# Performance work log

Hardware: AMD Instinct MI355X
Metric: run time of the kernel (lower is better)

## Reference

```python
import jax, jax.numpy as jnp
import numpy as np

B, S, D = 8, 512, 512
H, DK = 64, 8          # 64 heads hardcoded in SelfAttentiveLBLBiLM
WIDTH = 16             # local window width
NL = 2                 # highway layers
N = S + 2 * WIDTH      # padded sequence length


def setup_inputs() -> dict:
    key = jax.random.key(0)
    ks = jax.random.split(key, 12)
    s = 0.02
    return {
        "inputs": jax.random.normal(ks[0], (B, S, D), jnp.float32),
        "left_pad": jax.random.normal(ks[1], (WIDTH, D), jnp.float32) * s,
        "right_pad": jax.random.normal(ks[2], (WIDTH, D), jnp.float32) * s,
        "l_Wqkv": jax.random.normal(ks[3], (3, D, D), jnp.float32) * s,
        "l_bqkv": jnp.zeros((3, D), jnp.float32),
        "l_Wo": jax.random.normal(ks[4], (D, D), jnp.float32) * s,
        "l_bo": jnp.zeros((D,), jnp.float32),
        "r_Wqkv": jax.random.normal(ks[5], (3, D, D), jnp.float32) * s,
        "r_bqkv": jnp.zeros((3, D), jnp.float32),
        "r_Wo": jax.random.normal(ks[6], (D, D), jnp.float32) * s,
        "r_bo": jnp.zeros((D,), jnp.float32),
        "lhw_W": jax.random.normal(ks[7], (NL, 2 * D, D), jnp.float32) * s,
        "lhw_b": jnp.zeros((NL, 2 * D), jnp.float32),
        "rhw_W": jax.random.normal(ks[8], (NL, 2 * D, D), jnp.float32) * s,
        "rhw_b": jnp.zeros((NL, 2 * D), jnp.float32),
    }


def _masks(n, width):
    i = jnp.arange(n)[:, None]
    j = jnp.arange(n)[None, :]
    # local_mask: triu(k=-width-1) * (1 - triu(k=1)) -> i-width-1 <= j <= i
    left = (j <= i) & (j >= i - width - 1)
    # right mask is the full flip of the left mask
    right = (j >= i) & (j <= i + width + 1)
    return left, right


def _mha(x, Wqkv, bqkv, Wo, bo, mask):
    b, n, d = x.shape
    # torch Linear: y = x @ W.T + b, W is [out, in]
    qkv = jnp.einsum("bnd,tod->tbno", x, Wqkv) + bqkv[:, None, None, :]
    q, k, v = [t.reshape(b, n, H, DK).transpose(0, 2, 1, 3) for t in qkv]
    scores = jnp.einsum("bhqd,bhkd->bhqk", q, k) / jnp.sqrt(jnp.float32(DK))
    scores = jnp.where(mask[None, None], scores, jnp.float32(-1e9))
    p = jax.nn.softmax(scores, axis=-1)
    out = jnp.einsum("bhqk,bhkd->bhqd", p, v)
    out = out.transpose(0, 2, 1, 3).reshape(b, n, d)
    return out @ Wo.T + bo


def _highway(x, Ws, bs):
    for l in range(NL):
        proj = x @ Ws[l].T + bs[l]
        nonlin = jax.nn.relu(proj[..., :D])
        gate = jax.nn.sigmoid(proj[..., D:])
        x = gate * x + (1.0 - gate) * nonlin
    return x


def reference(inputs, left_pad, right_pad, l_Wqkv, l_bqkv, l_Wo, l_bo,
              r_Wqkv, r_bqkv, r_Wo, r_bo, lhw_W, lhw_b, rhw_W, rhw_b):
    b = inputs.shape[0]
    new_inputs = jnp.concatenate(
        [jnp.broadcast_to(left_pad[None], (b, WIDTH, D)), inputs,
         jnp.broadcast_to(right_pad[None], (b, WIDTH, D))], axis=1)  # [B, N, D]
    left_mask, right_mask = _masks(N, WIDTH)
    new_left = _mha(new_inputs, l_Wqkv, l_bqkv, l_Wo, l_bo, left_mask)
    new_right = _mha(new_inputs, r_Wqkv, r_bqkv, r_Wo, r_bo, right_mask)
    # per-step loop indexes position start + width -> slice [WIDTH : WIDTH + S]
    left_out = _highway(new_left[:, WIDTH:WIDTH + S], lhw_W, lhw_b)
    right_out = _highway(new_right[:, WIDTH:WIDTH + S], rhw_W, rhw_b)
    last = jnp.concatenate([left_out, right_out], axis=-1)  # [B, S, 2D]
    all_layers = last[None]  # [1, B, S, 2D] (single layer stacked on dim 0)
    return (all_layers, last)
```

## Files before the change

kernel.cpp:

```cpp
#include <hip/hip_runtime.h>
#include <math.h>

#define B_ 8
#define S_ 512
#define D_ 512
#define WIDTH_ 16
#define NSEQ 544
#define MROWS 4352
#define MOUT 4096
#define OUTHALF 4194304

typedef _Float16 half8 __attribute__((ext_vector_type(8)));
typedef _Float16 half4 __attribute__((ext_vector_type(4)));
typedef float floatx4 __attribute__((ext_vector_type(4)));

#define GLD16(g, l) __builtin_amdgcn_global_load_lds(                          \
    (const __attribute__((address_space(1))) void*)(g),                        \
    (__attribute__((address_space(3))) void*)(l), 16, 0, 0)

__device__ __forceinline__ float sigmoidf_(float x) {
    return 1.f / (1.f + __expf(-x));
}

__global__ __launch_bounds__(256)
void gemm_qkv(const _Float16* __restrict__ A,
              const _Float16* __restrict__ B0, const _Float16* __restrict__ B1,
              const float* __restrict__ bias0, const float* __restrict__ bias1,
              _Float16* __restrict__ C16) {
    const int lda = 512, ldb = 512, ldc = 1536, K = 512;
    __shared__ _Float16 As[128 * 32];
    __shared__ _Float16 Bs[128 * 32];
    const int t    = threadIdx.x;
    const int wave = t >> 6;
    const int lane = t & 63;
    const int bm = blockIdx.y * 128;
    const int bn = blockIdx.x * 128;
    const int z  = blockIdx.z;
    const _Float16* B = z ? B1 : B0;
    const float* bias = z ? bias1 : bias0;
    _Float16* C = C16 + (size_t)z * MROWS * 1536;
    const int wm = (wave & 1) * 64;
    const int wn = (wave >> 1) * 64;

    const int inst = wave * 2;
    const int r0 = inst * 16 + (lane >> 2);
    const int kf = (lane & 3) * 8;

    const _Float16* Ag0 = A + (size_t)(bm + r0) * lda + kf;
    const _Float16* Ag1 = Ag0 + (size_t)16 * lda;
    const _Float16* Bg0 = B + (size_t)(bn + r0) * ldb + kf;
    const _Float16* Bg1 = Bg0 + (size_t)16 * ldb;
    _Float16* As0 = &As[inst * 512];
    _Float16* As1 = As0 + 512;
    _Float16* Bs0 = &Bs[inst * 512];
    _Float16* Bs1 = Bs0 + 512;

    const int fr = lane & 15;
    const int fq = (lane >> 4) * 8;

    floatx4 acc[4][4] = {};

    for (int k0 = 0; k0 < K; k0 += 32) {
        GLD16(Ag0, As0); GLD16(Ag1, As1);
        GLD16(Bg0, Bs0); GLD16(Bg1, Bs1);
        Ag0 += 32; Ag1 += 32; Bg0 += 32; Bg1 += 32;
        __syncthreads();
        half8 af[4], bf[4];
#pragma unroll
        for (int s = 0; s < 4; s++) {
            af[s] = *(const half8*)&As[(wm + s * 16 + fr) * 32 + fq];
            bf[s] = *(const half8*)&Bs[(wn + s * 16 + fr) * 32 + fq];
        }
#pragma unroll
        for (int i = 0; i < 4; i++)
#pragma unroll
            for (int j = 0; j < 4; j++)
                acc[i][j] = __builtin_amdgcn_mfma_f32_16x16x32_f16(
                    af[i], bf[j], acc[i][j], 0, 0, 0);
        __syncthreads();
    }

    const int rq = (lane >> 4) * 4;
    const int cc = lane & 15;
#pragma unroll
    for (int i = 0; i < 4; i++) {
        const int rbase = bm + wm + i * 16 + rq;
#pragma unroll
        for (int j = 0; j < 4; j++) {
            const int col = bn + wn + j * 16 + cc;
            const float bv = bias[col];
#pragma unroll
            for (int r = 0; r < 4; r++)
                C[(size_t)(rbase + r) * ldc + col] = (_Float16)(acc[i][j][r] + bv);
        }
    }
}

__global__ __launch_bounds__(256)
void gemm_wo(const _Float16* __restrict__ Aall,
             const _Float16* __restrict__ B0, const _Float16* __restrict__ B1,
             const float* __restrict__ bias0, const float* __restrict__ bias1,
             _Float16* __restrict__ x16base) {
    const int lda = 512, ldb = 512, K = 512;
    __shared__ _Float16 As[64 * 32];
    __shared__ _Float16 Bs[128 * 32];
    const int t    = threadIdx.x;
    const int wave = t >> 6;
    const int lane = t & 63;
    const int bm = blockIdx.y * 64;
    const int bn = blockIdx.x * 128;
    const int z  = blockIdx.z;
    const _Float16* A = Aall + (size_t)z * MROWS * 512;
    const _Float16* B = z ? B1 : B0;
    const float* bias = z ? bias1 : bias0;
    _Float16* x16 = x16base + (size_t)z * MOUT * 512;

    const int wm = (wave & 1) * 32;
    const int wn = (wave >> 1) * 64;

    const int rA = wave * 16 + (lane >> 2);
    const int rB = wave * 32 + (lane >> 2);
    const int kf = (lane & 3) * 8;

    const _Float16* Ag0 = A + (size_t)(bm + rA) * lda + kf;
    const _Float16* Bg0 = B + (size_t)(bn + rB) * ldb + kf;
    const _Float16* Bg1 = Bg0 + (size_t)16 * ldb;
    _Float16* As0 = &As[wave * 512];
    _Float16* Bs0 = &Bs[wave * 1024];
    _Float16* Bs1 = Bs0 + 512;

    const int fr = lane & 15;
    const int fq = (lane >> 4) * 8;

    floatx4 acc[2][4] = {};

    for (int k0 = 0; k0 < K; k0 += 32) {
        GLD16(Ag0, As0);
        GLD16(Bg0, Bs0); GLD16(Bg1, Bs1);
        Ag0 += 32; Bg0 += 32; Bg1 += 32;
        __syncthreads();
        half8 af[2], bf[4];
#pragma unroll
        for (int s = 0; s < 2; s++)
            af[s] = *(const half8*)&As[(wm + s * 16 + fr) * 32 + fq];
#pragma unroll
        for (int s = 0; s < 4; s++)
            bf[s] = *(const half8*)&Bs[(wn + s * 16 + fr) * 32 + fq];
#pragma unroll
        for (int i = 0; i < 2; i++)
#pragma unroll
            for (int j = 0; j < 4; j++)
                acc[i][j] = __builtin_amdgcn_mfma_f32_16x16x32_f16(
                    af[i], bf[j], acc[i][j], 0, 0, 0);
        __syncthreads();
    }

    const int rq = (lane >> 4) * 4;
    const int cc = lane & 15;
#pragma unroll
    for (int i = 0; i < 2; i++) {
        const int rbase = bm + wm + i * 16 + rq;
#pragma unroll
        for (int r = 0; r < 4; r++) {
            const int row = rbase + r;
            const int b = row / NSEQ;
            const int s = row - b * NSEQ;
            if (s < WIDTH_ || s >= WIDTH_ + S_) continue;
            const int m = b * S_ + s - WIDTH_;
#pragma unroll
            for (int j = 0; j < 4; j++) {
                const int col = bn + wn + j * 16 + cc;
                x16[(size_t)m * 512 + col] = (_Float16)(acc[i][j][r] + bias[col]);
            }
        }
    }
}

__global__ __launch_bounds__(256)
void gemm_hw(const _Float16* __restrict__ x16inbase,
             const _Float16* __restrict__ W0, const _Float16* __restrict__ W1,
             const float* __restrict__ b0, const float* __restrict__ b1,
             _Float16* __restrict__ x16outbase,
             float* __restrict__ outlastbase,
             float* __restrict__ outallbase) {
    const int lda = 512, ldb = 512, K = 512;
    __shared__ _Float16 As[128 * 32];
    __shared__ _Float16 Bn[64 * 32];
    __shared__ _Float16 Bg[64 * 32];
    const int t    = threadIdx.x;
    const int wave = t >> 6;
    const int lane = t & 63;
    const int bm = blockIdx.y * 128;
    const int bn = blockIdx.x * 64;
    const int z  = blockIdx.z;
    const _Float16* A = x16inbase + (size_t)z * MOUT * 512;
    const _Float16* W = z ? W1 : W0;
    const float* bias = z ? b1 : b0;
    _Float16* x16out = x16outbase ? x16outbase + (size_t)z * MOUT * 512 : nullptr;

    const int wm = (wave & 1) * 64;
    const int wn = (wave >> 1) * 32;

    const int rA = wave * 32 + (lane >> 2);
    const int rB = wave * 16 + (lane >> 2);
    const int kf = (lane & 3) * 8;

    const _Float16* Ag0 = A + (size_t)(bm + rA) * lda + kf;
    const _Float16* Ag1 = Ag0 + (size_t)16 * lda;
    const _Float16* Bn0 = W + (size_t)(bn + rB) * ldb + kf;
    const _Float16* Bg0 = W + (size_t)(512 + bn + rB) * ldb + kf;
    _Float16* As0  = &As[wave * 1024];
    _Float16* As1  = As0 + 512;
    _Float16* Bns0 = &Bn[wave * 512];
    _Float16* Bgs0 = &Bg[wave * 512];

    const int fr = lane & 15;
    const int fq = (lane >> 4) * 8;

    floatx4 accn[4][2] = {};
    floatx4 accg[4][2] = {};

    for (int k0 = 0; k0 < K; k0 += 32) {
        GLD16(Ag0, As0); GLD16(Ag1, As1);
        GLD16(Bn0, Bns0);
        GLD16(Bg0, Bgs0);
        Ag0 += 32; Ag1 += 32; Bn0 += 32; Bg0 += 32;
        __syncthreads();
        half8 af[4], bnf[2], bgf[2];
#pragma unroll
        for (int s = 0; s < 4; s++)
            af[s] = *(const half8*)&As[(wm + s * 16 + fr) * 32 + fq];
#pragma unroll
        for (int s = 0; s < 2; s++) {
            bnf[s] = *(const half8*)&Bn[(wn + s * 16 + fr) * 32 + fq];
            bgf[s] = *(const half8*)&Bg[(wn + s * 16 + fr) * 32 + fq];
        }
#pragma unroll
        for (int i = 0; i < 4; i++)
#pragma unroll
            for (int j = 0; j < 2; j++) {
                accn[i][j] = __builtin_amdgcn_mfma_f32_16x16x32_f16(
                    af[i], bnf[j], accn[i][j], 0, 0, 0);
                accg[i][j] = __builtin_amdgcn_mfma_f32_16x16x32_f16(
                    af[i], bgf[j], accg[i][j], 0, 0, 0);
            }
        __syncthreads();
    }

    float* outlast = outlastbase ? outlastbase + z * 512 : nullptr;
    float* outall  = outallbase  ? outallbase  + z * 512 : nullptr;

    const int rq = (lane >> 4) * 4;
    const int cc = lane & 15;
#pragma unroll
    for (int i = 0; i < 4; i++) {
        const int rbase = bm + wm + i * 16 + rq;
#pragma unroll
        for (int j = 0; j < 2; j++) {
            const int col = bn + wn + j * 16 + cc;
            const float bnl = bias[col];
            const float bgt = bias[512 + col];
#pragma unroll
            for (int r = 0; r < 4; r++) {
                const int row = rbase + r;
                const float nl = fmaxf(accn[i][j][r] + bnl, 0.f);
                const float g  = sigmoidf_(accg[i][j][r] + bgt);
                const float xo = (float)A[(size_t)row * 512 + col];
                const float v  = g * xo + (1.f - g) * nl;
                if (x16out) {
                    x16out[(size_t)row * 512 + col] = (_Float16)v;
                } else {
                    outlast[(size_t)row * 1024 + col] = v;
                    outall[(size_t)row * 1024 + col] = v;
                }
            }
        }
    }
}

__global__ __launch_bounds__(256)
void attn_win(const _Float16* __restrict__ qkvall, _Float16* __restrict__ attall) {
    const int dir = blockIdx.y;
    const int dlo = dir ? 0 : -(WIDTH_ + 1);
    const _Float16* qkv = qkvall + (size_t)dir * MROWS * 1536;
    _Float16* att = attall + (size_t)dir * MROWS * 512;
    const int tid = blockIdx.x * 256 + threadIdx.x;
    const int h  = tid & 63;
    const int bi = tid >> 6;
    const int i  = bi % NSEQ;
    const int b  = bi / NSEQ;
    const int j0 = i + dlo;
    const float scale = 0.35355339059327373f;

    const half8 q8 = *(const half8*)(qkv + (size_t)bi * 1536 + h * 8);
    float q[8];
#pragma unroll
    for (int d = 0; d < 8; d++) q[d] = (float)q8[d];

    float s[18];
    float mx = -1e30f;
#pragma unroll
    for (int jj = 0; jj < 18; jj++) {
        const int j = j0 + jj;
        const int jc = j < 0 ? 0 : (j > NSEQ - 1 ? NSEQ - 1 : j);
        const half8 k8 = *(const half8*)(qkv + (size_t)(b * NSEQ + jc) * 1536 + 512 + h * 8);
        float d = 0.f;
#pragma unroll
        for (int dd = 0; dd < 8; dd++) d = fmaf(q[dd], (float)k8[dd], d);
        s[jj] = (j == jc) ? d * scale : -1e30f;
        mx = fmaxf(mx, s[jj]);
    }
    float sum = 0.f;
#pragma unroll
    for (int jj = 0; jj < 18; jj++) { s[jj] = __expf(s[jj] - mx); sum += s[jj]; }
    const float inv = 1.f / sum;

    float o[8] = {};
#pragma unroll
    for (int jj = 0; jj < 18; jj++) {
        const int j = j0 + jj;
        const int jc = j < 0 ? 0 : (j > NSEQ - 1 ? NSEQ - 1 : j);
        const half8 v8 = *(const half8*)(qkv + (size_t)(b * NSEQ + jc) * 1536 + 1024 + h * 8);
        const float p = s[jj];
#pragma unroll
        for (int dd = 0; dd < 8; dd++) o[dd] = fmaf(p, (float)v8[dd], o[dd]);
    }
    half8 o16;
#pragma unroll
    for (int d = 0; d < 8; d++) o16[d] = (_Float16)(o[d] * inv);
    *(half8*)&att[(size_t)bi * 512 + h * 8] = o16;
}

__global__ void prep(const float* __restrict__ lq, const float* __restrict__ rq,
                     const float* __restrict__ lo, const float* __restrict__ ro,
                     const float* __restrict__ lh, const float* __restrict__ rh,
                     _Float16* __restrict__ wdst,
                     const float* __restrict__ inp,
                     const float* __restrict__ lp,
                     const float* __restrict__ rp,
                     _Float16* __restrict__ padX) {
    const int gb = blockIdx.x;
    if (gb < 4096) {
        int idx = gb * 256 + threadIdx.x;
        const float* src; int off;
        if      (idx < 196608) { src = lq; off = idx; }
        else if (idx < 393216) { src = rq; off = idx - 196608; }
        else if (idx < 458752) { src = lo; off = idx - 393216; }
        else if (idx < 524288) { src = ro; off = idx - 458752; }
        else if (idx < 786432) { src = lh; off = idx - 524288; }
        else                   { src = rh; off = idx - 786432; }
        const float4 v = ((const float4*)src)[off];
        half4 h = { (_Float16)v.x, (_Float16)v.y, (_Float16)v.z, (_Float16)v.w };
        ((half4*)wdst)[idx] = h;
    } else {
        int idx = (gb - 4096) * 256 + threadIdx.x;
        const int c4 = idx & 127;
        const int t  = idx >> 7;
        const int n = t % NSEQ;
        const int b = t / NSEQ;
        const float* src;
        if (n < WIDTH_)            src = lp + n * 512;
        else if (n < WIDTH_ + S_)  src = inp + ((size_t)(b * S_ + n - WIDTH_)) * 512;
        else                       src = rp + (n - WIDTH_ - S_) * 512;
        const float4 v = *(const float4*)(src + c4 * 4);
        half4 h = { (_Float16)v.x, (_Float16)v.y, (_Float16)v.z, (_Float16)v.w };
        *(half4*)&padX[(size_t)t * 512 + c4 * 4] = h;
    }
}

extern "C" void kernel_launch(void* const* d_in, const int* in_sizes, int n_in,
                              void* d_out, int out_size, void* d_ws, size_t ws_size,
                              hipStream_t stream) {
    const float* inputs    = (const float*)d_in[0];
    const float* left_pad  = (const float*)d_in[1];
    const float* right_pad = (const float*)d_in[2];
    const float* l_Wqkv = (const float*)d_in[3];
    const float* l_bqkv = (const float*)d_in[4];
    const float* l_Wo   = (const float*)d_in[5];
    const float* l_bo   = (const float*)d_in[6];
    const float* r_Wqkv = (const float*)d_in[7];
    const float* r_bqkv = (const float*)d_in[8];
    const float* r_Wo   = (const float*)d_in[9];
    const float* r_bo   = (const float*)d_in[10];
    const float* lhw_W  = (const float*)d_in[11];
    const float* lhw_b  = (const float*)d_in[12];
    const float* rhw_W  = (const float*)d_in[13];
    const float* rhw_b  = (const float*)d_in[14];

    float* out = (float*)d_out;
    _Float16* h = (_Float16*)d_ws;

    _Float16* padX16 = h;
    _Float16* w16    = h + 2228224;
    _Float16* lqkv16 = w16;
    _Float16* rqkv16 = w16 + 786432;
    _Float16* lWo16  = w16 + 1572864;
    _Float16* rWo16  = w16 + 1835008;
    _Float16* lhw16  = w16 + 2097152;
    _Float16* rhw16  = w16 + 3145728;
    _Float16* qkv16  = h + 6422528;
    _Float16* att16  = h + 19791872;
    _Float16* x16a   = h + 24248320;
    _Float16* x16b   = h + 28442624;

    float* out_all  = out;
    float* out_last = out + OUTHALF;

    prep<<<6272, 256, 0, stream>>>(l_Wqkv, r_Wqkv, l_Wo, r_Wo, lhw_W, rhw_W, w16,
                                   inputs, left_pad, right_pad, padX16);

    gemm_qkv<<<dim3(12, 34, 2), 256, 0, stream>>>(
        padX16, lqkv16, rqkv16, l_bqkv, r_bqkv, qkv16);

    attn_win<<<dim3(MROWS * 64 / 256, 2), 256, 0, stream>>>(qkv16, att16);

    gemm_wo<<<dim3(4, 68, 2), 256, 0, stream>>>(
        att16, lWo16, rWo16, l_bo, r_bo, x16a);

    gemm_hw<<<dim3(8, 32, 2), 256, 0, stream>>>(
        x16a, lhw16, rhw16, lhw_b, rhw_b, x16b, nullptr, nullptr);
    gemm_hw<<<dim3(8, 32, 2), 256, 0, stream>>>(
        x16b, lhw16 + 524288, rhw16 + 524288, lhw_b + 1024, rhw_b + 1024,
        nullptr, out_last, out_all);
}
```

Measured before the change: 220.6 us.

## Fuse all stages into a persistent megakernel with grid-wide barriers

Replaces the six separate kernel launches with one persistent kernel of 512 blocks that loops over each stage's work items and separates stages with a software global barrier built on atomics. This is meant to remove launch overhead and the idle gaps between kernels. In exchange, each stage is now limited to 512 resident blocks, which reduces parallelism for stages that had more blocks. The barrier assumes all blocks are co-resident and adds spin-wait cost, and a memset is added to reset the barrier counter.

New measurement: 712.5 us. 3.23x slower.

```diff
diff --git a/kernel.cpp b/kernel.cpp
--- a/kernel.cpp
+++ b/kernel.cpp
@@ -9,6 +9,7 @@
 #define MROWS 4352
 #define MOUT 4096
 #define OUTHALF 4194304
+#define NBLK 512
 
 typedef _Float16 half8 __attribute__((ext_vector_type(8)));
 typedef _Float16 half4 __attribute__((ext_vector_type(4)));
@@ -22,404 +23,435 @@
     return 1.f / (1.f + __expf(-x));
 }
 
-__global__ __launch_bounds__(256)
-void gemm_qkv(const _Float16* __restrict__ A,
-              const _Float16* __restrict__ B0, const _Float16* __restrict__ B1,
-              const float* __restrict__ bias0, const float* __restrict__ bias1,
-              _Float16* __restrict__ C16) {
+struct Args {
+    const float *inputs, *left_pad, *right_pad;
+    const float *l_Wqkv, *l_bqkv, *l_Wo, *l_bo;
+    const float *r_Wqkv, *r_bqkv, *r_Wo, *r_bo;
+    const float *lhw_W, *lhw_b, *rhw_W, *rhw_b;
+    _Float16 *padX16, *w16;
+    _Float16 *lqkv16, *rqkv16, *lWo16, *rWo16, *lhw16, *rhw16;
+    _Float16 *qkv16, *att16, *x16a, *x16b;
+    float *out_all, *out_last;
+    int *bar;
+};
+
+__device__ __forceinline__ void gsync(int* bar, int tid) {
+    __syncthreads();
+    if (tid == 0) {
+        int* cnt = bar;
+        int* gen = bar + 1;
+        const int g = __hip_atomic_load(gen, __ATOMIC_RELAXED, __HIP_MEMORY_SCOPE_AGENT);
+        const int prev = __hip_atomic_fetch_add(cnt, 1, __ATOMIC_ACQ_REL, __HIP_MEMORY_SCOPE_AGENT);
+        if (prev == NBLK - 1) {
+            __hip_atomic_store(cnt, 0, __ATOMIC_RELAXED, __HIP_MEMORY_SCOPE_AGENT);
+            __hip_atomic_fetch_add(gen, 1, __ATOMIC_RELEASE, __HIP_MEMORY_SCOPE_AGENT);
+        } else {
+            while (__hip_atomic_load(gen, __ATOMIC_ACQUIRE, __HIP_MEMORY_SCOPE_AGENT) == g)
+                __builtin_amdgcn_s_sleep(8);
+        }
+    }
+    __syncthreads();
+}
+
+__device__ __forceinline__ void prep_phase(const Args& a, int pb, int tid) {
+    for (int gb = pb; gb < 6272; gb += NBLK) {
+        if (gb < 4096) {
+            int idx = gb * 256 + tid;
+            const float* src; int off;
+            if      (idx < 196608) { src = a.l_Wqkv; off = idx; }
+            else if (idx < 393216) { src = a.r_Wqkv; off = idx - 196608; }
+            else if (idx < 458752) { src = a.l_Wo;   off = idx - 393216; }
+            else if (idx < 524288) { src = a.r_Wo;   off = idx - 458752; }
+            else if (idx < 786432) { src = a.lhw_W;  off = idx - 524288; }
+            else                   { src = a.rhw_W;  off = idx - 786432; }
+            const float4 v = ((const float4*)src)[off];
+            half4 h = { (_Float16)v.x, (_Float16)v.y, (_Float16)v.z, (_Float16)v.w };
+            ((half4*)a.w16)[idx] = h;
+        } else {
+            int idx = (gb - 4096) * 256 + tid;
+            const int c4 = idx & 127;
+            const int t  = idx >> 7;
+            const int n = t % NSEQ;
+            const int b = t / NSEQ;
+            const float* src;
+            if (n < WIDTH_)            src = a.left_pad + n * 512;
+            else if (n < WIDTH_ + S_)  src = a.inputs + ((size_t)(b * S_ + n - WIDTH_)) * 512;
+            else                       src = a.right_pad + (n - WIDTH_ - S_) * 512;
+            const float4 v = *(const float4*)(src + c4 * 4);
+            half4 h = { (_Float16)v.x, (_Float16)v.y, (_Float16)v.z, (_Float16)v.w };
+            *(half4*)&a.padX16[(size_t)t * 512 + c4 * 4] = h;
+        }
+    }
+}
+
+__device__ __forceinline__ void qkv_phase(const Args& a, int pb, int tid,
+                                          _Float16* As, _Float16* Bs) {
     const int lda = 512, ldb = 512, ldc = 1536, K = 512;
-    __shared__ _Float16 As[128 * 32];
-    __shared__ _Float16 Bs[128 * 32];
-    const int t    = threadIdx.x;
-    const int wave = t >> 6;
-    const int lane = t & 63;
-    const int bm = blockIdx.y * 128;
-    const int bn = blockIdx.x * 128;
-    const int z  = blockIdx.z;
-    const _Float16* B = z ? B1 : B0;
-    const float* bias = z ? bias1 : bias0;
-    _Float16* C = C16 + (size_t)z * MROWS * 1536;
-    const int wm = (wave & 1) * 64;
-    const int wn = (wave >> 1) * 64;
-
-    const int inst = wave * 2;
-    const int r0 = inst * 16 + (lane >> 2);
-    const int kf = (lane & 3) * 8;
-
-    const _Float16* Ag0 = A + (size_t)(bm + r0) * lda + kf;
-    const _Float16* Ag1 = Ag0 + (size_t)16 * lda;
-    const _Float16* Bg0 = B + (size_t)(bn + r0) * ldb + kf;
-    const _Float16* Bg1 = Bg0 + (size_t)16 * ldb;
-    _Float16* As0 = &As[inst * 512];
-    _Float16* As1 = As0 + 512;
-    _Float16* Bs0 = &Bs[inst * 512];
-    _Float16* Bs1 = Bs0 + 512;
-
-    const int fr = lane & 15;
-    const int fq = (lane >> 4) * 8;
-
-    floatx4 acc[4][4] = {};
-
-    for (int k0 = 0; k0 < K; k0 += 32) {
-        GLD16(Ag0, As0); GLD16(Ag1, As1);
-        GLD16(Bg0, Bs0); GLD16(Bg1, Bs1);
-        Ag0 += 32; Ag1 += 32; Bg0 += 32; Bg1 += 32;
-        __syncthreads();
-        half8 af[4], bf[4];
-#pragma unroll
-        for (int s = 0; s < 4; s++) {
-            af[s] = *(const half8*)&As[(wm + s * 16 + fr) * 32 + fq];
-            bf[s] = *(const half8*)&Bs[(wn + s * 16 + fr) * 32 + fq];
-        }
-#pragma unroll
-        for (int i = 0; i < 4; i++)
-#pragma unroll
-            for (int j = 0; j < 4; j++)
-                acc[i][j] = __builtin_amdgcn_mfma_f32_16x16x32_f16(
-                    af[i], bf[j], acc[i][j], 0, 0, 0);
-        __syncthreads();
-    }
-
-    const int rq = (lane >> 4) * 4;
-    const int cc = lane & 15;
-#pragma unroll
-    for (int i = 0; i < 4; i++) {
-        const int rbase = bm + wm + i * 16 + rq;
-#pragma unroll
-        for (int j = 0; j < 4; j++) {
-            const int col = bn + wn + j * 16 + cc;
-            const float bv = bias[col];
-#pragma unroll
-            for (int r = 0; r < 4; r++)
-                C[(size_t)(rbase + r) * ldc + col] = (_Float16)(acc[i][j][r] + bv);
-        }
-    }
-}
-
-__global__ __launch_bounds__(256)
-void gemm_wo(const _Float16* __restrict__ Aall,
-             const _Float16* __restrict__ B0, const _Float16* __restrict__ B1,
-             const float* __restrict__ bias0, const float* __restrict__ bias1,
-             _Float16* __restrict__ x16base) {
-    const int lda = 512, ldb = 512, K = 512;
-    __shared__ _Float16 As[64 * 32];
-    __shared__ _Float16 Bs[128 * 32];
-    const int t    = threadIdx.x;
-    const int wave = t >> 6;
-    const int lane = t & 63;
-    const int bm = blockIdx.y * 64;
-    const int bn = blockIdx.x * 128;
-    const int z  = blockIdx.z;
-    const _Float16* A = Aall + (size_t)z * MROWS * 512;
-    const _Float16* B = z ? B1 : B0;
-    const float* bias = z ? bias1 : bias0;
-    _Float16* x16 = x16base + (size_t)z * MOUT * 512;
-
-    const int wm = (wave & 1) * 32;
-    const int wn = (wave >> 1) * 64;
-
-    const int rA = wave * 16 + (lane >> 2);
-    const int rB = wave * 32 + (lane >> 2);
-    const int kf = (lane & 3) * 8;
-
-    const _Float16* Ag0 = A + (size_t)(bm + rA) * lda + kf;
-    const _Float16* Bg0 = B + (size_t)(bn + rB) * ldb + kf;
-    const _Float16* Bg1 = Bg0 + (size_t)16 * ldb;
-    _Float16* As0 = &As[wave * 512];
-    _Float16* Bs0 = &Bs[wave * 1024];
-    _Float16* Bs1 = Bs0 + 512;
-
-    const int fr = lane & 15;
-    const int fq = (lane >> 4) * 8;
-
-    floatx4 acc[2][4] = {};
-
-    for (int k0 = 0; k0 < K; k0 += 32) {
-        GLD16(Ag0, As0);
-        GLD16(Bg0, Bs0); GLD16(Bg1, Bs1);
-        Ag0 += 32; Bg0 += 32; Bg1 += 32;
-        __syncthreads();
-        half8 af[2], bf[4];
-#pragma unroll
-        for (int s = 0; s < 2; s++)
-            af[s] = *(const half8*)&As[(wm + s * 16 + fr) * 32 + fq];
-#pragma unroll
-        for (int s = 0; s < 4; s++)
-            bf[s] = *(const half8*)&Bs[(wn + s * 16 + fr) * 32 + fq];
-#pragma unroll
-        for (int i = 0; i < 2; i++)
-#pragma unroll
-            for (int j = 0; j < 4; j++)
-                acc[i][j] = __builtin_amdgcn_mfma_f32_16x16x32_f16(
-                    af[i], bf[j], acc[i][j], 0, 0, 0);
-        __syncthreads();
-    }
-
-    const int rq = (lane >> 4) * 4;
-    const int cc = lane & 15;
-#pragma unroll
-    for (int i = 0; i < 2; i++) {
-        const int rbase = bm + wm + i * 16 + rq;
-#pragma unroll
-        for (int r = 0; r < 4; r++) {
-            const int row = rbase + r;
-            const int b = row / NSEQ;
-            const int s = row - b * NSEQ;
-            if (s < WIDTH_ || s >= WIDTH_ + S_) continue;
-            const int m = b * S_ + s - WIDTH_;
+    const int wave = tid >> 6;
+    const int lane = tid & 63;
+    for (int job = pb; job < 816; job += NBLK) {
+        const int z   = job / 408;
+        const int rem = job % 408;
+        const int bm  = (rem / 12) * 128;
+        const int bn  = (rem % 12) * 128;
+        const _Float16* A = a.padX16;
+        const _Float16* B = z ? a.rqkv16 : a.lqkv16;
+        const float* bias = z ? a.r_bqkv : a.l_bqkv;
+        _Float16* C = a.qkv16 + (size_t)z * MROWS * 1536;
+        const int wm = (wave & 1) * 64;
+        const int wn = (wave >> 1) * 64;
+
+        const int inst = wave * 2;
+        const int r0 = inst * 16 + (lane >> 2);
+        const int kf = (lane & 3) * 8;
+
+        const _Float16* Ag0 = A + (size_t)(bm + r0) * lda + kf;
+        const _Float16* Ag1 = Ag0 + (size_t)16 * lda;
+        const _Float16* Bg0 = B + (size_t)(bn + r0) * ldb + kf;
+        const _Float16* Bg1 = Bg0 + (size_t)16 * ldb;
+        _Float16* As0 = &As[inst * 512];
+        _Float16* As1 = As0 + 512;
+        _Float16* Bs0 = &Bs[inst * 512];
+        _Float16* Bs1 = Bs0 + 512;
+
+        const int fr = lane & 15;
+        const int fq = (lane >> 4) * 8;
+
+        floatx4 acc[4][4] = {};
+
+        for (int k0 = 0; k0 < K; k0 += 32) {
+            GLD16(Ag0, As0); GLD16(Ag1, As1);
+            GLD16(Bg0, Bs0); GLD16(Bg1, Bs1);
+            Ag0 += 32; Ag1 += 32; Bg0 += 32; Bg1 += 32;
+            __syncthreads();
+            half8 af[4], bf[4];
+#pragma unroll
+            for (int s = 0; s < 4; s++) {
+                af[s] = *(const half8*)&As[(wm + s * 16 + fr) * 32 + fq];
+                bf[s] = *(const half8*)&Bs[(wn + s * 16 + fr) * 32 + fq];
+            }
+#pragma unroll
+            for (int i = 0; i < 4; i++)
+#pragma unroll
+                for (int j = 0; j < 4; j++)
+                    acc[i][j] = __builtin_amdgcn_mfma_f32_16x16x32_f16(
+                        af[i], bf[j], acc[i][j], 0, 0, 0);
+            __syncthreads();
+        }
+
+        const int rq = (lane >> 4) * 4;
+        const int cc = lane & 15;
+#pragma unroll
+        for (int i = 0; i < 4; i++) {
+            const int rbase = bm + wm + i * 16 + rq;
 #pragma unroll
             for (int j = 0; j < 4; j++) {
                 const int col = bn + wn + j * 16 + cc;
-                x16[(size_t)m * 512 + col] = (_Float16)(acc[i][j][r] + bias[col]);
+                const float bv = bias[col];
+#pragma unroll
+                for (int r = 0; r < 4; r++)
+                    C[(size_t)(rbase + r) * ldc + col] = (_Float16)(acc[i][j][r] + bv);
             }
         }
     }
 }
 
-__global__ __launch_bounds__(256)
-void gemm_hw(const _Float16* __restrict__ x16inbase,
-             const _Float16* __restrict__ W0, const _Float16* __restrict__ W1,
-             const float* __restrict__ b0, const float* __restrict__ b1,
-             _Float16* __restrict__ x16outbase,
-             float* __restrict__ outlastbase,
-             float* __restrict__ outallbase) {
+__device__ __forceinline__ void attn_phase(const Args& a, int pb, int tid) {
+    for (int job = pb; job < 2176; job += NBLK) {
+        const int dir = job / 1088;
+        const int jx  = job % 1088;
+        const int dlo = dir ? 0 : -(WIDTH_ + 1);
+        const _Float16* qkv = a.qkv16 + (size_t)dir * MROWS * 1536;
+        _Float16* att = a.att16 + (size_t)dir * MROWS * 512;
+        const int t  = jx * 256 + tid;
+        const int h  = t & 63;
+        const int bi = t >> 6;
+        const int i  = bi % NSEQ;
+        const int b  = bi / NSEQ;
+        const int j0 = i + dlo;
+        const float scale = 0.35355339059327373f;
+
+        const half8 q8 = *(const half8*)(qkv + (size_t)bi * 1536 + h * 8);
+        float q[8];
+#pragma unroll
+        for (int d = 0; d < 8; d++) q[d] = (float)q8[d];
+
+        float s[18];
+        float mx = -1e30f;
+#pragma unroll
+        for (int jj = 0; jj < 18; jj++) {
+            const int j = j0 + jj;
+            const int jc = j < 0 ? 0 : (j > NSEQ - 1 ? NSEQ - 1 : j);
+            const half8 k8 = *(const half8*)(qkv + (size_t)(b * NSEQ + jc) * 1536 + 512 + h * 8);
+            float d = 0.f;
+#pragma unroll
+            for (int dd = 0; dd < 8; dd++) d = fmaf(q[dd], (float)k8[dd], d);
+            s[jj] = (j == jc) ? d * scale : -1e30f;
+            mx = fmaxf(mx, s[jj]);
+        }
+        float sum = 0.f;
+#pragma unroll
+        for (int jj = 0; jj < 18; jj++) { s[jj] = __expf(s[jj] - mx); sum += s[jj]; }
+        const float inv = 1.f / sum;
+
+        float o[8] = {};
+#pragma unroll
+        for (int jj = 0; jj < 18; jj++) {
+            const int j = j0 + jj;
+            const int jc = j < 0 ? 0 : (j > NSEQ - 1 ? NSEQ - 1 : j);
+            const half8 v8 = *(const half8*)(qkv + (size_t)(b * NSEQ + jc) * 1536 + 1024 + h * 8);
+            const float p = s[jj];
+#pragma unroll
+            for (int dd = 0; dd < 8; dd++) o[dd] = fmaf(p, (float)v8[dd], o[dd]);
+        }
+        half8 o16;
+#pragma unroll
+        for (int d = 0; d < 8; d++) o16[d] = (_Float16)(o[d] * inv);
+        *(half8*)&att[(size_t)bi * 512 + h * 8] = o16;
+    }
+}
+
+__device__ __forceinline__ void wo_phase(const Args& a, int pb, int tid,
+                                         _Float16* As, _Float16* Bs) {
     const int lda = 512, ldb = 512, K = 512;
-    __shared__ _Float16 As[128 * 32];
-    __shared__ _Float16 Bn[64 * 32];
-    __shared__ _Float16 Bg[64 * 32];
-    const int t    = threadIdx.x;
-    const int wave = t >> 6;
-    const int lane = t & 63;
-    const int bm = blockIdx.y * 128;
-    const int bn = blockIdx.x * 64;
-    const int z  = blockIdx.z;
-    const _Float16* A = x16inbase + (size_t)z * MOUT * 512;
-    const _Float16* W = z ? W1 : W0;
-    const float* bias = z ? b1 : b0;
-    _Float16* x16out = x16outbase ? x16outbase + (size_t)z * MOUT * 512 : nullptr;
-
-    const int wm = (wave & 1) * 64;
-    const int wn = (wave >> 1) * 32;
-
-    const int rA = wave * 32 + (lane >> 2);
-    const int rB = wave * 16 + (lane >> 2);
-    const int kf = (lane & 3) * 8;
-
-    const _Float16* Ag0 = A + (size_t)(bm + rA) * lda + kf;
-    const _Float16* Ag1 = Ag0 + (size_t)16 * lda;
-    const _Float16* Bn0 = W + (size_t)(bn + rB) * ldb + kf;
-    const _Float16* Bg0 = W + (size_t)(512 + bn + rB) * ldb + kf;
-    _Float16* As0  = &As[wave * 1024];
-    _Float16* As1  = As0 + 512;
-    _Float16* Bns0 = &Bn[wave * 512];
-    _Float16* Bgs0 = &Bg[wave * 512];
-
-    const int fr = lane & 15;
-    const int fq = (lane >> 4) * 8;
-
-    floatx4 accn[4][2] = {};
-    floatx4 accg[4][2] = {};
-
-    for (int k0 = 0; k0 < K; k0 += 32) {
-        GLD16(Ag0, As0); GLD16(Ag1, As1);
-        GLD16(Bn0, Bns0);
-        GLD16(Bg0, Bgs0);
-        Ag0 += 32; Ag1 += 32; Bn0 += 32; Bg0 += 32;
-        __syncthreads();
-        half8 af[4], bnf[2], bgf[2];
-#pragma unroll
-        for (int s = 0; s < 4; s++)
-            af[s] = *(const half8*)&As[(wm + s * 16 + fr) * 32 + fq];
-#pragma unroll
-        for (int s = 0; s < 2; s++) {
-            bnf[s] = *(const half8*)&Bn[(wn + s * 16 + fr) * 32 + fq];
-            bgf[s] = *(const half8*)&Bg[(wn + s * 16 + fr) * 32 + fq];
-        }
-#pragma unroll
-        for (int i = 0; i < 4; i++)
-#pragma unroll
-            for (int j = 0; j < 2; j++) {
-                accn[i][j] = __builtin_amdgcn_mfma_f32_16x16x32_f16(
-                    af[i], bnf[j], accn[i][j], 0, 0, 0);
-                accg[i][j] = __builtin_amdgcn_mfma_f32_16x16x32_f16(
-                    af[i], bgf[j], accg[i][j], 0, 0, 0);
-            }
-        __syncthreads();
-    }
-
-    float* outlast = outlastbase ? outlastbase + z * 512 : nullptr;
-    float* outall  = outallbase  ? outallbase  + z * 512 : nullptr;
-
-    const int rq = (lane >> 4) * 4;
-    const int cc = lane & 15;
-#pragma unroll
-    for (int i = 0; i < 4; i++) {
-        const int rbase = bm + wm + i * 16 + rq;
-#pragma unroll
-        for (int j = 0; j < 2; j++) {
-            const int col = bn + wn + j * 16 + cc;
-            const float bnl = bias[col];
-            const float bgt = bias[512 + col];
+    const int wave = tid >> 6;
+    const int lane = tid & 63;
+    for (int job = pb; job < 544; job += NBLK) {
+        const int z   = job / 272;
+        const int rem = job % 272;
+        const int bm  = (rem / 4) * 64;
+        const int bn  = (rem % 4) * 128;
+        const _Float16* A = a.att16 + (size_t)z * MROWS * 512;
+        const _Float16* B = z ? a.rWo16 : a.lWo16;
+        const float* bias = z ? a.r_bo : a.l_bo;
+        _Float16* x16 = a.x16a + (size_t)z * MOUT * 512;
+
+        const int wm = (wave & 1) * 32;
+        const int wn = (wave >> 1) * 64;
+
+        const int rA = wave * 16 + (lane >> 2);
+        const int rB = wave * 32 + (lane >> 2);
+        const int kf = (lane & 3) * 8;
+
+        const _Float16* Ag0 = A + (size_t)(bm + rA) * lda + kf;
+        const _Float16* Bg0 = B + (size_t)(bn + rB) * ldb + kf;
+        const _Float16* Bg1 = Bg0 + (size_t)16 * ldb;
+        _Float16* As0 = &As[wave * 512];
+        _Float16* Bs0 = &Bs[wave * 1024];
+        _Float16* Bs1 = Bs0 + 512;
+
+        const int fr = lane & 15;
+        const int fq = (lane >> 4) * 8;
+
+        floatx4 acc[2][4] = {};
+
+        for (int k0 = 0; k0 < K; k0 += 32) {
+            GLD16(Ag0, As0);
+            GLD16(Bg0, Bs0); GLD16(Bg1, Bs1);
+            Ag0 += 32; Bg0 += 32; Bg1 += 32;
+            __syncthreads();
+            half8 af[2], bf[4];
+#pragma unroll
+            for (int s = 0; s < 2; s++)
+                af[s] = *(const half8*)&As[(wm + s * 16 + fr) * 32 + fq];
+#pragma unroll
+            for (int s = 0; s < 4; s++)
+                bf[s] = *(const half8*)&Bs[(wn + s * 16 + fr) * 32 + fq];
+#pragma unroll
+            for (int i = 0; i < 2; i++)
+#pragma unroll
+                for (int j = 0; j < 4; j++)
+                    acc[i][j] = __builtin_amdgcn_mfma_f32_16x16x32_f16(
+                        af[i], bf[j], acc[i][j], 0, 0, 0);
+            __syncthreads();
+        }
+
+        const int rq = (lane >> 4) * 4;
+        const int cc = lane & 15;
+#pragma unroll
+        for (int i = 0; i < 2; i++) {
+            const int rbase = bm + wm + i * 16 + rq;
 #pragma unroll
             for (int r = 0; r < 4; r++) {
                 const int row = rbase + r;
-                const float nl = fmaxf(accn[i][j][r] + bnl, 0.f);
-                const float g  = sigmoidf_(accg[i][j][r] + bgt);
-                const float xo = (float)A[(size_t)row * 512 + col];
-                const float v  = g * xo + (1.f - g) * nl;
-                if (x16out) {
-                    x16out[(size_t)row * 512 + col] = (_Float16)v;
-                } else {
-                    outlast[(size_t)row * 1024 + col] = v;
-                    outall[(size_t)row * 1024 + col] = v;
+                const int b = row / NSEQ;
+                const int s = row - b * NSEQ;
+                if (s < WIDTH_ || s >= WIDTH_ + S_) continue;
+                const int m = b * S_ + s - WIDTH_;
+#pragma unroll
+                for (int j = 0; j < 4; j++) {
+                    const int col = bn + wn + j * 16 + cc;
+                    x16[(size_t)m * 512 + col] = (_Float16)(acc[i][j][r] + bias[col]);
                 }
             }
         }
     }
 }
 
-__global__ __launch_bounds__(256)
-void attn_win(const _Float16* __restrict__ qkvall, _Float16* __restrict__ attall) {
-    const int dir = blockIdx.y;
-    const int dlo = dir ? 0 : -(WIDTH_ + 1);
-    const _Float16* qkv = qkvall + (size_t)dir * MROWS * 1536;
-    _Float16* att = attall + (size_t)dir * MROWS * 512;
-    const int tid = blockIdx.x * 256 + threadIdx.x;
-    const int h  = tid & 63;
-    const int bi = tid >> 6;
-    const int i  = bi % NSEQ;
-    const int b  = bi / NSEQ;
-    const int j0 = i + dlo;
-    const float scale = 0.35355339059327373f;
-
-    const half8 q8 = *(const half8*)(qkv + (size_t)bi * 1536 + h * 8);
-    float q[8];
-#pragma unroll
-    for (int d = 0; d < 8; d++) q[d] = (float)q8[d];
-
-    float s[18];
-    float mx = -1e30f;
-#pragma unroll
-    for (int jj = 0; jj < 18; jj++) {
-        const int j = j0 + jj;
-        const int jc = j < 0 ? 0 : (j > NSEQ - 1 ? NSEQ - 1 : j);
-        const half8 k8 = *(const half8*)(qkv + (size_t)(b * NSEQ + jc) * 1536 + 512 + h * 8);
-        float d = 0.f;
-#pragma unroll
-        for (int dd = 0; dd < 8; dd++) d = fmaf(q[dd], (float)k8[dd], d);
-        s[jj] = (j == jc) ? d * scale : -1e30f;
-        mx = fmaxf(mx, s[jj]);
-    }
-    float sum = 0.f;
-#pragma unroll
-    for (int jj = 0; jj < 18; jj++) { s[jj] = __expf(s[jj] - mx); sum += s[jj]; }
-    const float inv = 1.f / sum;
-
-    float o[8] = {};
-#pragma unroll
-    for (int jj = 0; jj < 18; jj++) {
-        const int j = j0 + jj;
-        const int jc = j < 0 ? 0 : (j > NSEQ - 1 ? NSEQ - 1 : j);
-        const half8 v8 = *(const half8*)(qkv + (size_t)(b * NSEQ + jc) * 1536 + 1024 + h * 8);
-        const float p = s[jj];
-#pragma unroll
-        for (int dd = 0; dd < 8; dd++) o[dd] = fmaf(p, (float)v8[dd], o[dd]);
-    }
-    half8 o16;
-#pragma unroll
-    for (int d = 0; d < 8; d++) o16[d] = (_Float16)(o[d] * inv);
-    *(half8*)&att[(size_t)bi * 512 + h * 8] = o16;
-}
-
-__global__ void prep(const float* __restrict__ lq, const float* __restrict__ rq,
-                     const float* __restrict__ lo, const float* __restrict__ ro,
-                     const float* __restrict__ lh, const float* __restrict__ rh,
-                     _Float16* __restrict__ wdst,
-                     const float* __restrict__ inp,
-                     const float* __restrict__ lp,
-                     const float* __restrict__ rp,
-                     _Float16* __restrict__ padX) {
-    const int gb = blockIdx.x;
-    if (gb < 4096) {
-        int idx = gb * 256 + threadIdx.x;
-        const float* src; int off;
-        if      (idx < 196608) { src = lq; off = idx; }
-        else if (idx < 393216) { src = rq; off = idx - 196608; }
-        else if (idx < 458752) { src = lo; off = idx - 393216; }
-        else if (idx < 524288) { src = ro; off = idx - 458752; }
-        else if (idx < 786432) { src = lh; off = idx - 524288; }
-        else                   { src = rh; off = idx - 786432; }
-        const float4 v = ((const float4*)src)[off];
-        half4 h = { (_Float16)v.x, (_Float16)v.y, (_Float16)v.z, (_Float16)v.w };
-        ((half4*)wdst)[idx] = h;
-    } else {
-        int idx = (gb - 4096) * 256 + threadIdx.x;
-        const int c4 = idx & 127;
-        const int t  = idx >> 7;
-        const int n = t % NSEQ;
-        const int b = t / NSEQ;
-        const float* src;
-        if (n < WIDTH_)            src = lp + n * 512;
-        else if (n < WIDTH_ + S_)  src = inp + ((size_t)(b * S_ + n - WIDTH_)) * 512;
-        else                       src = rp + (n - WIDTH_ - S_) * 512;
-        const float4 v = *(const float4*)(src + c4 * 4);
-        half4 h = { (_Float16)v.x, (_Float16)v.y, (_Float16)v.z, (_Float16)v.w };
-        *(half4*)&padX[(size_t)t * 512 + c4 * 4] = h;
-    }
+__device__ __forceinline__ void hw_phase(const Args& a, int pb, int tid,
+                                         _Float16* As, _Float16* Bn, _Float16* Bg,
+                                         const _Float16* x16inbase,
+                                         const _Float16* W0, const _Float16* W1,
+                                         const float* b0, const float* b1,
+                                         _Float16* x16outbase,
+                                         float* outlastbase, float* outallbase) {
+    const int lda = 512, ldb = 512, K = 512;
+    const int wave = tid >> 6;
+    const int lane = tid & 63;
+    for (int job = pb; job < 512; job += NBLK) {
+        const int z   = job / 256;
+        const int rem = job % 256;
+        const int bm  = (rem / 8) * 128;
+        const int bn  = (rem % 8) * 64;
+        const _Float16* A = x16inbase + (size_t)z * MOUT * 512;
+        const _Float16* W = z ? W1 : W0;
+        const float* bias = z ? b1 : b0;
+        _Float16* x16out = x16outbase ? x16outbase + (size_t)z * MOUT * 512 : nullptr;
+
+        const int wm = (wave & 1) * 64;
+        const int wn = (wave >> 1) * 32;
+
+        const int rA = wave * 32 + (lane >> 2);
+        const int rB = wave * 16 + (lane >> 2);
+        const int kf = (lane & 3) * 8;
+
+        const _Float16* Ag0 = A + (size_t)(bm + rA) * lda + kf;
+        const _Float16* Ag1 = Ag0 + (size_t)16 * lda;
+        const _Float16* Bn0 = W + (size_t)(bn + rB) * ldb + kf;
+        const _Float16* Bg0 = W + (size_t)(512 + bn + rB) * ldb + kf;
+        _Float16* As0  = &As[wave * 1024];
+        _Float16* As1  = As0 + 512;
+        _Float16* Bns0 = &Bn[wave * 512];
+        _Float16* Bgs0 = &Bg[wave * 512];
+
+        const int fr = lane & 15;
+        const int fq = (lane >> 4) * 8;
+
+        floatx4 accn[4][2] = {};
+        floatx4 accg[4][2] = {};
+
+        for (int k0 = 0; k0 < K; k0 += 32) {
+            GLD16(Ag0, As0); GLD16(Ag1, As1);
+            GLD16(Bn0, Bns0);
+            GLD16(Bg0, Bgs0);
+            Ag0 += 32; Ag1 += 32; Bn0 += 32; Bg0 += 32;
+            __syncthreads();
+            half8 af[4], bnf[2], bgf[2];
+#pragma unroll
+            for (int s = 0; s < 4; s++)
+                af[s] = *(const half8*)&As[(wm + s * 16 + fr) * 32 + fq];
+#pragma unroll
+            for (int s = 0; s < 2; s++) {
+                bnf[s] = *(const half8*)&Bn[(wn + s * 16 + fr) * 32 + fq];
+                bgf[s] = *(const half8*)&Bg[(wn + s * 16 + fr) * 32 + fq];
+            }
+#pragma unroll
+            for (int i = 0; i < 4; i++)
+#pragma unroll
+                for (int j = 0; j < 2; j++) {
+                    accn[i][j] = __builtin_amdgcn_mfma_f32_16x16x32_f16(
+                        af[i], bnf[j], accn[i][j], 0, 0, 0);
+                    accg[i][j] = __builtin_amdgcn_mfma_f32_16x16x32_f16(
+                        af[i], bgf[j], accg[i][j], 0, 0, 0);
+                }
+            __syncthreads();
+        }
+
+        float* outlast = outlastbase ? outlastbase + z * 512 : nullptr;
+        float* outall  = outallbase  ? outallbase  + z * 512 : nullptr;
+
+        const int rq = (lane >> 4) * 4;
+        const int cc = lane & 15;
+#pragma unroll
+        for (int i = 0; i < 4; i++) {
+            const int rbase = bm + wm + i * 16 + rq;
+#pragma unroll
+            for (int j = 0; j < 2; j++) {
+                const int col = bn + wn + j * 16 + cc;
+                const float bnl = bias[col];
+                const float bgt = bias[512 + col];
+#pragma unroll
+                for (int r = 0; r < 4; r++) {
+                    const int row = rbase + r;
+                    const float nl = fmaxf(accn[i][j][r] + bnl, 0.f);
+                    const float g  = sigmoidf_(accg[i][j][r] + bgt);
+                    const float xo = (float)A[(size_t)row * 512 + col];
+                    const float v  = g * xo + (1.f - g) * nl;
+                    if (x16out) {
+                        x16out[(size_t)row * 512 + col] = (_Float16)v;
+                    } else {
+                        outlast[(size_t)row * 1024 + col] = v;
+                        outall[(size_t)row * 1024 + col] = v;
+                    }
+                }
+            }
+        }
+    }
+}
+
+__global__ void __launch_bounds__(256, 2) mega(Args a) {
+    __shared__ _Float16 S[8192];
+    const int pb  = blockIdx.x;
+    const int tid = threadIdx.x;
+
+    prep_phase(a, pb, tid);
+    gsync(a.bar, tid);
+    qkv_phase(a, pb, tid, S, S + 4096);
+    gsync(a.bar, tid);
+    attn_phase(a, pb, tid);
+    gsync(a.bar, tid);
+    wo_phase(a, pb, tid, S, S + 2048);
+    gsync(a.bar, tid);
+    hw_phase(a, pb, tid, S, S + 4096, S + 6144,
+             a.x16a, a.lhw16, a.rhw16, a.lhw_b, a.rhw_b,
+             a.x16b, nullptr, nullptr);
+    gsync(a.bar, tid);
+    hw_phase(a, pb, tid, S, S + 4096, S + 6144,
+             a.x16b, a.lhw16 + 524288, a.rhw16 + 524288,
+             a.lhw_b + 1024, a.rhw_b + 1024,
+             nullptr, a.out_last, a.out_all);
 }
 
 extern "C" void kernel_launch(void* const* d_in, const int* in_sizes, int n_in,
                               void* d_out, int out_size, void* d_ws, size_t ws_size,
                               hipStream_t stream) {
-    const float* inputs    = (const float*)d_in[0];
-    const float* left_pad  = (const float*)d_in[1];
-    const float* right_pad = (const float*)d_in[2];
-    const float* l_Wqkv = (const float*)d_in[3];
-    const float* l_bqkv = (const float*)d_in[4];
-    const float* l_Wo   = (const float*)d_in[5];
-    const float* l_bo   = (const float*)d_in[6];
-    const float* r_Wqkv = (const float*)d_in[7];
-    const float* r_bqkv = (const float*)d_in[8];
-    const float* r_Wo   = (const float*)d_in[9];
-    const float* r_bo   = (const float*)d_in[10];
-    const float* lhw_W  = (const float*)d_in[11];
-    const float* lhw_b  = (const float*)d_in[12];
-    const float* rhw_W  = (const float*)d_in[13];
-    const float* rhw_b  = (const float*)d_in[14];
-
     float* out = (float*)d_out;
     _Float16* h = (_Float16*)d_ws;
 
-    _Float16* padX16 = h;
-    _Float16* w16    = h + 2228224;
-    _Float16* lqkv16 = w16;
-    _Float16* rqkv16 = w16 + 786432;
-    _Float16* lWo16  = w16 + 1572864;
-    _Float16* rWo16  = w16 + 1835008;
-    _Float16* lhw16  = w16 + 2097152;
-    _Float16* rhw16  = w16 + 3145728;
-    _Float16* qkv16  = h + 6422528;
-    _Float16* att16  = h + 19791872;
-    _Float16* x16a   = h + 24248320;
-    _Float16* x16b   = h + 28442624;
-
-    float* out_all  = out;
-    float* out_last = out + OUTHALF;
-
-    prep<<<6272, 256, 0, stream>>>(l_Wqkv, r_Wqkv, l_Wo, r_Wo, lhw_W, rhw_W, w16,
-                                   inputs, left_pad, right_pad, padX16);
-
-    gemm_qkv<<<dim3(12, 34, 2), 256, 0, stream>>>(
-        padX16, lqkv16, rqkv16, l_bqkv, r_bqkv, qkv16);
-
-    attn_win<<<dim3(MROWS * 64 / 256, 2), 256, 0, stream>>>(qkv16, att16);
-
-    gemm_wo<<<dim3(4, 68, 2), 256, 0, stream>>>(
-        att16, lWo16, rWo16, l_bo, r_bo, x16a);
-
-    gemm_hw<<<dim3(8, 32, 2), 256, 0, stream>>>(
-        x16a, lhw16, rhw16, lhw_b, rhw_b, x16b, nullptr, nullptr);
-    gemm_hw<<<dim3(8, 32, 2), 256, 0, stream>>>(
-        x16b, lhw16 + 524288, rhw16 + 524288, lhw_b + 1024, rhw_b + 1024,
-        nullptr, out_last, out_all);
-}
+    Args a;
+    a.inputs    = (const float*)d_in[0];
+    a.left_pad  = (const float*)d_in[1];
+    a.right_pad = (const float*)d_in[2];
+    a.l_Wqkv = (const float*)d_in[3];
+    a.l_bqkv = (const float*)d_in[4];
+    a.l_Wo   = (const float*)d_in[5];
+    a.l_bo   = (const float*)d_in[6];
+    a.r_Wqkv = (const float*)d_in[7];
+    a.r_bqkv = (const float*)d_in[8];
+    a.r_Wo   = (const float*)d_in[9];
+    a.r_bo   = (const float*)d_in[10];
+    a.lhw_W  = (const float*)d_in[11];
+    a.lhw_b  = (const float*)d_in[12];
+    a.rhw_W  = (const float*)d_in[13];
+    a.rhw_b  = (const float*)d_in[14];
+
+    a.padX16 = h;
+    a.w16    = h + 2228224;
+    a.lqkv16 = a.w16;
+    a.rqkv16 = a.w16 + 786432;
+    a.lWo16  = a.w16 + 1572864;
+    a.rWo16  = a.w16 + 1835008;
+    a.lhw16  = a.w16 + 2097152;
+    a.rhw16  = a.w16 + 3145728;
+    a.qkv16  = h + 6422528;
+    a.att16  = h + 19791872;
+    a.x16a   = h + 24248320;
+    a.x16b   = h + 28442624;
+    a.out_all  = out;
+    a.out_last = out + OUTHALF;
+
+    a.bar = (int*)((char*)d_ws + ((ws_size - 64) & ~(size_t)63));
+
+    hipMemsetAsync(a.bar, 0, 8, stream);
+    mega<<<dim3(NBLK), dim3(256), 0, stream>>>(a);
+}
```
